# Performance work log

Hardware: AMD Instinct MI355X
Metric: run time of the kernel (lower is better)

Reference implementation:

```python
import jax, jax.numpy as jnp
import numpy as np

N_NODES = 100000
N_EDGES = 1600000
DROP_P = 0.5  # F.dropout default, training=True by default in the source
LRELU_SLOPE = 0.01
EPS = 1e-12


def setup_inputs() -> dict:
    key = jax.random.key(0)
    ks = jax.random.split(key, 8)
    x = jax.random.normal(ks[0], (N_NODES, 64), dtype=jnp.float32)
    edge_index = jax.random.randint(ks[1], (2, N_EDGES), 0, N_NODES, dtype=jnp.int64)
    s = 1.0 / np.sqrt(64)
    W1_l = jax.random.uniform(ks[2], (64, 32), jnp.float32, -s, s)
    W1_r = jax.random.uniform(ks[3], (64, 32), jnp.float32, -s, s)
    b1 = jnp.zeros((32,), jnp.float32)
    s2 = 1.0 / np.sqrt(32)
    W2_l = jax.random.uniform(ks[4], (32, 64), jnp.float32, -s2, s2)
    W2_r = jax.random.uniform(ks[5], (32, 64), jnp.float32, -s2, s2)
    b2 = jnp.zeros((64,), jnp.float32)
    return {"x": x, "edge_index": edge_index, "W1_l": W1_l, "b1": b1,
            "W1_r": W1_r, "W2_l": W2_l, "b2": b2, "W2_r": W2_r}


def _sage_conv(x, src, dst, W_l, b, W_r, n):
    # mean aggregation of source features onto destinations (PyG SAGEConv)
    msg = x[src]                                                 # [E, d]
    agg = jax.ops.segment_sum(msg, dst, num_segments=n)          # [N, d]
    cnt = jax.ops.segment_sum(jnp.ones((src.shape[0],), x.dtype), dst, num_segments=n)
    mean = agg / jnp.maximum(cnt, 1.0)[:, None]
    return mean @ W_l + b + x @ W_r


def _dropout(x, key):
    keep = jax.random.bernoulli(key, 1.0 - DROP_P, x.shape)
    return jnp.where(keep, x / (1.0 - DROP_P), 0.0).astype(x.dtype)


def reference(x, edge_index, W1_l, b1, W1_r, W2_l, b2, W2_r):
    n = x.shape[0]
    src, dst = edge_index[0], edge_index[1]
    dk = jax.random.split(jax.random.key(42), 2)
    h = _sage_conv(x, src, dst, W1_l, b1, W1_r, n)
    h = jax.nn.leaky_relu(h, LRELU_SLOPE)
    h = _dropout(h, dk[0])
    h = _sage_conv(h, src, dst, W2_l, b2, W2_r, n)
    h = _dropout(h, dk[1])
    norm = jnp.sqrt(jnp.sum(h * h, axis=1, keepdims=True))
    return h / jnp.maximum(norm, EPS)
```

## Files before the change

### kernel.cpp

```cpp
#include <hip/hip_runtime.h>

#define N_NODES 100000
#define N_EDGES 1600000
#define NPB 32
#define NB (N_NODES / NPB)
#define CAP 704
#define NCC 49
#define CAPA 34816
#define NFB 64
#define BPC 16
#define N16 (N_NODES * 16)
#define GHB 6250
#define M1W 50000
#define M2W 100000

typedef float v2f __attribute__((ext_vector_type(2)));

#define PIN4(v) asm volatile("" : "+v"(v.x), "+v"(v.y), "+v"(v.z), "+v"(v.w))

struct U2 { unsigned a, b; };

__host__ __device__ constexpr U2 tf2x32(unsigned k0, unsigned k1, unsigned c0, unsigned c1) {
  unsigned ks2 = k0 ^ k1 ^ 0x1BD11BDAu;
  unsigned x0 = c0 + k0, x1 = c1 + k1;
#define TFR(r) { x0 += x1; x1 = (x1 << (r)) | (x1 >> (32 - (r))); x1 ^= x0; }
  TFR(13) TFR(15) TFR(26) TFR(6)
  x0 += k1;  x1 += ks2 + 1u;
  TFR(17) TFR(29) TFR(16) TFR(24)
  x0 += ks2; x1 += k0 + 2u;
  TFR(13) TFR(15) TFR(26) TFR(6)
  x0 += k0;  x1 += k1 + 3u;
  TFR(17) TFR(29) TFR(16) TFR(24)
  x0 += k1;  x1 += ks2 + 4u;
  TFR(13) TFR(15) TFR(26) TFR(6)
  x0 += ks2; x1 += k0 + 5u;
#undef TFR
  return U2{x0, x1};
}

constexpr U2 DK0 = tf2x32(0u, 42u, 0u, 0u);
constexpr U2 DK1 = tf2x32(0u, 42u, 0u, 1u);

__device__ __forceinline__ bool keep_bit(unsigned k0, unsigned k1, unsigned j) {
  U2 w = tf2x32(k0, k1, 0u, j);
  return ((w.a ^ w.b) >> 31) == 0u;
}

__device__ __forceinline__ unsigned short f2bf(float f) {
  unsigned u = __float_as_uint(f);
  u += 0x7FFFu + ((u >> 16) & 1u);
  return (unsigned short)(u >> 16);
}
__device__ __forceinline__ v2f up2(unsigned r) {
  v2f v;
  v.x = __uint_as_float(r << 16);
  v.y = __uint_as_float(r & 0xFFFF0000u);
  return v;
}

__device__ __forceinline__ float4 ldcol(const float* __restrict__ W, int i,
                                        int lane, int ld) {
  float4 v;
  v.x = W[(i * 4 + 0) * ld + lane];
  v.y = W[(i * 4 + 1) * ld + lane];
  v.z = W[(i * 4 + 2) * ld + lane];
  v.w = W[(i * 4 + 3) * ld + lane];
  return v;
}

__global__ __launch_bounds__(256) void k_mask(unsigned long long* __restrict__ msk) {
  int w = (int)((blockIdx.x * blockDim.x + threadIdx.x) >> 6);
  int lane = threadIdx.x & 63;
  int nw = (int)((gridDim.x * blockDim.x) >> 6);
  for (; w < M1W + M2W; w += nw) {
    unsigned k0, k1, j;
    if (w < M1W) { k0 = DK0.a; k1 = DK0.b; j = (unsigned)w * 64u + (unsigned)lane; }
    else { k0 = DK1.a; k1 = DK1.b; j = (unsigned)(w - M1W) * 64u + (unsigned)lane; }
    unsigned long long bits = __ballot(keep_bit(k0, k1, j));
    if (lane == 0) msk[w] = bits;
  }
}

__global__ __launch_bounds__(256, 4) void k_transform1(
    const float* __restrict__ x, const float* __restrict__ Wl,
    const float* __restrict__ Wr, unsigned short* __restrict__ xlbh,
    float* __restrict__ xr) {
  __shared__ __align__(16) float rv[2][4][64];
  int lane = threadIdx.x & 63;
  int wv = (threadIdx.x >> 6) & 3;
  const float* W = (lane < 32) ? Wl : Wr;
  int c = lane & 31;
  float4 V0 = ldcol(W, 0, c, 32);   PIN4(V0);
  float4 V1 = ldcol(W, 1, c, 32);   PIN4(V1);
  float4 V2 = ldcol(W, 2, c, 32);   PIN4(V2);
  float4 V3 = ldcol(W, 3, c, 32);   PIN4(V3);
  float4 V4 = ldcol(W, 4, c, 32);   PIN4(V4);
  float4 V5 = ldcol(W, 5, c, 32);   PIN4(V5);
  float4 V6 = ldcol(W, 6, c, 32);   PIN4(V6);
  float4 V7 = ldcol(W, 7, c, 32);   PIN4(V7);
  float4 V8 = ldcol(W, 8, c, 32);   PIN4(V8);
  float4 V9 = ldcol(W, 9, c, 32);   PIN4(V9);
  float4 V10 = ldcol(W, 10, c, 32); PIN4(V10);
  float4 V11 = ldcol(W, 11, c, 32); PIN4(V11);
  float4 V12 = ldcol(W, 12, c, 32); PIN4(V12);
  float4 V13 = ldcol(W, 13, c, 32); PIN4(V13);
  float4 V14 = ldcol(W, 14, c, 32); PIN4(V14);
  float4 V15 = ldcol(W, 15, c, 32); PIN4(V15);
  int wid0 = (int)((blockIdx.x * blockDim.x + threadIdx.x) >> 6);
  int wstride = (int)((gridDim.x * blockDim.x) >> 6);
  float xv = x[wid0 * 64 + lane];
  int b = 0;
  for (int wid = wid0; wid < N_NODES; wid += wstride) {
    rv[b][wv][lane] = xv;
    int nxt = wid + wstride;
    if (nxt < N_NODES) xv = x[nxt * 64 + lane];
    asm volatile("s_waitcnt lgkmcnt(0)" ::: "memory");
    const float* rb = &rv[b][wv][0];
    v2f s0 = {0.f, 0.f}, s1 = {0.f, 0.f};
#define TST(Vi, i) { \
    float4 r = *(const float4*)(rb + (i) * 4); \
    v2f w0; w0.x = Vi.x; w0.y = Vi.y; \
    v2f w1; w1.x = Vi.z; w1.y = Vi.w; \
    v2f p0; p0.x = r.x; p0.y = r.y; \
    v2f p1; p1.x = r.z; p1.y = r.w; \
    s0 += p0 * w0; s1 += p1 * w1; }
    TST(V0, 0)  TST(V1, 1)  TST(V2, 2)  TST(V3, 3)
    TST(V4, 4)  TST(V5, 5)  TST(V6, 6)  TST(V7, 7)
    TST(V8, 8)  TST(V9, 9)  TST(V10, 10) TST(V11, 11)
    TST(V12, 12) TST(V13, 13) TST(V14, 14) TST(V15, 15)
#undef TST
    float s = (s0.x + s0.y) + (s1.x + s1.y);
    if (lane < 32) xlbh[(size_t)(c >> 4) * N16 + wid * 16 + (c & 15)] = f2bf(s);
    else           xr[wid * 32 + c] = s;
    b ^= 1;
  }
}

__global__ __launch_bounds__(256) void k_binA(
    const int* __restrict__ src, const int* __restrict__ dst,
    int* __restrict__ curA, unsigned* __restrict__ bufA) {
  __shared__ int hist[NCC];
  __shared__ int offsL[NCC + 1];
  __shared__ int baseL[NCC];
  __shared__ int place[NCC];
  __shared__ unsigned stag[2048];
  __shared__ unsigned char cellb[2048];
  int t = threadIdx.x;
  for (long long start = (long long)blockIdx.x * 2048; start < N_EDGES;
       start += (long long)gridDim.x * 2048) {
    int n = (int)min((long long)2048, (long long)N_EDGES - start);
    for (int i = t; i < NCC; i += 256) hist[i] = 0;
    __syncthreads();
    unsigned pv[8]; int pc[8];
#pragma unroll
    for (int i = 0; i < 8; ++i) {
      int idx = t + i * 256;
      if (idx < n) {
        int d = dst[start + idx];
        int s = src[start + idx];
        int cc = d >> 11;
        pc[i] = cc;
        pv[i] = (unsigned)s | ((unsigned)(d & 2047) << 17);
        atomicAdd(&hist[cc], 1);
      } else pc[i] = -1;
    }
    __syncthreads();
    if (t < 64) {
      int lane = t;
      int v = (lane < NCC) ? hist[lane] : 0;
      int x = v;
#pragma unroll
      for (int o = 1; o < 64; o <<= 1) {
        int y = __shfl_up(x, o, 64);
        if (lane >= o) x += y;
      }
      if (lane < NCC) {
        offsL[lane] = x - v;
        place[lane] = 0;
        if (v > 0) baseL[lane] = atomicAdd(&curA[lane], v);
      }
      if (lane == NCC - 1) offsL[NCC] = x;
    }
    __syncthreads();
#pragma unroll
    for (int i = 0; i < 8; ++i) {
      if (pc[i] >= 0) {
        int p = atomicAdd(&place[pc[i]], 1);
        int sl = offsL[pc[i]] + p;
        stag[sl] = pv[i];
        cellb[sl] = (unsigned char)pc[i];
      }
    }
    __syncthreads();
    for (int s2 = t; s2 < n; s2 += 256) {
      int cell = cellb[s2];
      int pos = baseL[cell] + (s2 - offsL[cell]);
      if (pos < CAPA) bufA[(size_t)cell * CAPA + pos] = stag[s2];
    }
    __syncthreads();
  }
}

__global__ __launch_bounds__(256) void k_binB(
    const unsigned* __restrict__ bufA, const int* __restrict__ curA,
    int* __restrict__ cur, unsigned* __restrict__ buf) {
  __shared__ int hist[NFB];
  __shared__ int offsL[NFB + 1];
  __shared__ int baseL[NFB];
  __shared__ int place[NFB];
  __shared__ unsigned stag[2048];
  __shared__ unsigned char cellb[2048];
  int cellc = blockIdx.x / BPC;
  int slice = blockIdx.x % BPC;
  int t = threadIdx.x;
  int cnt = min(curA[cellc], CAPA);
  const unsigned* in = bufA + (size_t)cellc * CAPA;
  for (int start = slice * 2048; start < cnt; start += BPC * 2048) {
    int n = min(2048, cnt - start);
    for (int i = t; i < NFB; i += 256) hist[i] = 0;
    __syncthreads();
    unsigned pv[8]; int pb[8];
#pragma unroll
    for (int i = 0; i < 8; ++i) {
      int idx = t + i * 256;
      if (idx < n) {
        unsigned w = in[start + idx];
        int dlow = (int)(w >> 17);
        int fb = dlow >> 5;
        pb[i] = fb;
        pv[i] = (w & 0x1FFFFu) | ((unsigned)(dlow & 31) << 17);
        atomicAdd(&hist[fb], 1);
      } else pb[i] = -1;
    }
    __syncthreads();
    if (t < 64) {
      int lane = t;
      int v = hist[lane];
      int x = v;
#pragma unroll
      for (int o = 1; o < 64; o <<= 1) {
        int y = __shfl_up(x, o, 64);
        if (lane >= o) x += y;
      }
      offsL[lane] = x - v;
      place[lane] = 0;
      if (v > 0) baseL[lane] = atomicAdd(&cur[cellc * NFB + lane], v);
      if (lane == 63) offsL[NFB] = x;
    }
    __syncthreads();
#pragma unroll
    for (int i = 0; i < 8; ++i) {
      if (pb[i] >= 0) {
        int p = atomicAdd(&place[pb[i]], 1);
        int sl = offsL[pb[i]] + p;
        stag[sl] = pv[i];
        cellb[sl] = (unsigned char)pb[i];
      }
    }
    __syncthreads();
    for (int s2 = t; s2 < n; s2 += 256) {
      int fb = cellb[s2];
      int pos = baseL[fb] + (s2 - offsL[fb]);
      if (pos < CAP) buf[(size_t)(cellc * NFB + fb) * CAP + pos] = stag[s2];
    }
    __syncthreads();
  }
}

__global__ __launch_bounds__(1024) void k_bscan(
    const int* __restrict__ cur, int* __restrict__ bbase) {
  __shared__ int warp_sums[16];
  __shared__ int s_running;
  int t = threadIdx.x;
  int lane = t & 63, w = t >> 6;
  if (t == 0) s_running = 0;
  __syncthreads();
  for (int base = 0; base < NB; base += 1024) {
    int i = base + t;
    int v = (i < NB) ? min(cur[i], CAP) : 0;
    int x = v;
#pragma unroll
    for (int o = 1; o < 64; o <<= 1) {
      int y = __shfl_up(x, o, 64);
      if (lane >= o) x += y;
    }
    if (lane == 63) warp_sums[w] = x;
    __syncthreads();
    if (w == 0) {
      int ws = (lane < 16) ? warp_sums[lane] : 0;
#pragma unroll
      for (int o = 1; o < 16; o <<= 1) {
        int y = __shfl_up(ws, o, 64);
        if (lane >= o) ws += y;
      }
      if (lane < 16) warp_sums[lane] = ws;
    }
    __syncthreads();
    int incl = x + (w > 0 ? warp_sums[w - 1] : 0);
    int excl = s_running + incl - v;
    if (i < NB) bbase[i] = excl;
    __syncthreads();
    if (t == 1023) s_running += incl;
    __syncthreads();
  }
}

__global__ __launch_bounds__(256) void k_bfill(
    const unsigned* __restrict__ buf, const int* __restrict__ cur,
    const int* __restrict__ bbase, int* __restrict__ deg,
    int* __restrict__ offs, int* __restrict__ eidx) {
  __shared__ int ncnt[NPB];
  __shared__ int ncur[NPB];
  __shared__ unsigned sbuf[CAP];
  int b = blockIdx.x, t = threadIdx.x;
  if (t < NPB) ncnt[t] = 0;
  __syncthreads();
  int nb = min(cur[b], CAP);
  const unsigned* bb = buf + (size_t)b * CAP;
  for (int slot = t; slot < nb; slot += 256) {
    unsigned w = bb[slot];
    sbuf[slot] = w;
    atomicAdd(&ncnt[w >> 17], 1);
  }
  __syncthreads();
  if (t < 64) {
    int lane = t;
    int c = (lane < NPB) ? ncnt[lane] : 0;
    int x = c;
#pragma unroll
    for (int o = 1; o < 32; o <<= 1) {
      int y = __shfl_up(x, o, 64);
      if (lane >= o) x += y;
    }
    if (lane < NPB) {
      int excl = x - c;
      ncur[lane] = excl;
      int gn = b * NPB + lane;
      deg[gn] = c;
      offs[gn] = bbase[b] + excl;
    }
  }
  __syncthreads();
  int base = bbase[b];
  for (int slot = t; slot < nb; slot += 256) {
    unsigned w = sbuf[slot];
    int p = atomicAdd(&ncur[w >> 17], 1);
    eidx[base + p] = (int)(w & 0x1FFFF);
  }
}

__global__ __launch_bounds__(256) void k_gather1(
    const unsigned short* __restrict__ xlbh, const float* __restrict__ xr,
    const int* __restrict__ offs, const int* __restrict__ deg,
    const int* __restrict__ eidx, const float* __restrict__ b1,
    const unsigned long long* __restrict__ msk1,
    unsigned short* __restrict__ hpbh) {
  int bb = blockIdx.x;
  int G = 0, nb = bb;
  if (nb >= GHB) { G = 1; nb -= GHB; }
  int tid = threadIdx.x;
  int lane = tid & 63;
  int node = nb * 16 + (tid >> 4);
  int g = (tid >> 2) & 3;
  int ch = tid & 3;
  int c = tid & 15;
  int col = G * 16 + c;
  int off = offs[node];
  int dg = deg[node];
  float xr_v = xr[node * 32 + col];
  float b1_v = b1[col];
  unsigned jj = (unsigned)(node * 32 + col);
  unsigned long long mw = msk1[jj >> 6];
  const uint2* H = (const uint2*)(xlbh + (size_t)G * N16);
  v2f acc01 = {0.f, 0.f}, acc23 = {0.f, 0.f};
  int k = 0;
  for (; k + 8 <= dg; k += 8) {
    int s0 = eidx[off + k + g];
    int s1 = eidx[off + k + 4 + g];
    uint2 r0 = H[s0 * 4 + ch];
    uint2 r1 = H[s1 * 4 + ch];
    acc01 += up2(r0.x); acc23 += up2(r0.y);
    acc01 += up2(r1.x); acc23 += up2(r1.y);
  }
  for (; k < dg; k += 4) {
    if (k + g < dg) {
      int s = eidx[off + k + g];
      uint2 r = H[s * 4 + ch];
      acc01 += up2(r.x); acc23 += up2(r.y);
    }
  }
  float a0 = acc01.x, a1 = acc01.y, a2 = acc23.x, a3 = acc23.y;
  a0 += __shfl_xor(a0, 4, 64); a0 += __shfl_xor(a0, 8, 64);
  a1 += __shfl_xor(a1, 4, 64); a1 += __shfl_xor(a1, 8, 64);
  a2 += __shfl_xor(a2, 4, 64); a2 += __shfl_xor(a2, 8, 64);
  a3 += __shfl_xor(a3, 4, 64); a3 += __shfl_xor(a3, 8, 64);
  int srcl = (lane & 48) + (c >> 2);
  float t0 = __shfl(a0, srcl, 64);
  float t1 = __shfl(a1, srcl, 64);
  float t2 = __shfl(a2, srcl, 64);
  float t3 = __shfl(a3, srcl, 64);
  int sub = lane & 3;
  float val = (sub == 0) ? t0 : (sub == 1) ? t1 : (sub == 2) ? t2 : t3;
  float inv = 1.0f / fmaxf((float)dg, 1.0f);
  float v = val * inv + b1_v + xr_v;
  v = (v > 0.f) ? v : 0.01f * v;
  float h = ((mw >> (jj & 63)) & 1ull) ? 2.0f * v : 0.0f;
  hpbh[(size_t)G * N16 + node * 16 + c] = f2bf(h);
}

__global__ __launch_bounds__(256) void k_gather2(
    const unsigned short* __restrict__ hpbh, const int* __restrict__ offs,
    const int* __restrict__ deg, const int* __restrict__ eidx,
    float* __restrict__ aggh) {
  int bb = blockIdx.x;
  int G = 0, nb = bb;
  if (nb >= GHB) { G = 1; nb -= GHB; }
  int tid = threadIdx.x;
  int lane = tid & 63;
  int node = nb * 16 + (tid >> 4);
  int g = (tid >> 2) & 3;
  int ch = tid & 3;
  int c = tid & 15;
  int off = offs[node];
  int dg = deg[node];
  const uint2* H = (const uint2*)(hpbh + (size_t)G * N16);
  v2f acc01 = {0.f, 0.f}, acc23 = {0.f, 0.f};
  int k = 0;
  for (; k + 8 <= dg; k += 8) {
    int s0 = eidx[off + k + g];
    int s1 = eidx[off + k + 4 + g];
    uint2 r0 = H[s0 * 4 + ch];
    uint2 r1 = H[s1 * 4 + ch];
    acc01 += up2(r0.x); acc23 += up2(r0.y);
    acc01 += up2(r1.x); acc23 += up2(r1.y);
  }
  for (; k < dg; k += 4) {
    if (k + g < dg) {
      int s = eidx[off + k + g];
      uint2 r = H[s * 4 + ch];
      acc01 += up2(r.x); acc23 += up2(r.y);
    }
  }
  float a0 = acc01.x, a1 = acc01.y, a2 = acc23.x, a3 = acc23.y;
  a0 += __shfl_xor(a0, 4, 64); a0 += __shfl_xor(a0, 8, 64);
  a1 += __shfl_xor(a1, 4, 64); a1 += __shfl_xor(a1, 8, 64);
  a2 += __shfl_xor(a2, 4, 64); a2 += __shfl_xor(a2, 8, 64);
  a3 += __shfl_xor(a3, 4, 64); a3 += __shfl_xor(a3, 8, 64);
  int srcl = (lane & 48) + (c >> 2);
  float t0 = __shfl(a0, srcl, 64);
  float t1 = __shfl(a1, srcl, 64);
  float t2 = __shfl(a2, srcl, 64);
  float t3 = __shfl(a3, srcl, 64);
  int sub = lane & 3;
  float val = (sub == 0) ? t0 : (sub == 1) ? t1 : (sub == 2) ? t2 : t3;
  float inv = 1.0f / fmaxf((float)dg, 1.0f);
  aggh[(size_t)G * N16 + node * 16 + c] = val * inv;
}

__global__ __launch_bounds__(256, 4) void k_out2(
    const unsigned short* __restrict__ hpbh, const float* __restrict__ aggh,
    const float* __restrict__ W2l, const float* __restrict__ b2,
    const float* __restrict__ W2r, const unsigned long long* __restrict__ msk2,
    float* __restrict__ out) {
  __shared__ __align__(16) float rv[2][4][64];
  int lane = threadIdx.x & 63;
  int wv = (threadIdx.x >> 6) & 3;
  float4 L0 = ldcol(W2l, 0, lane, 64); PIN4(L0);
  float4 L1 = ldcol(W2l, 1, lane, 64); PIN4(L1);
  float4 L2 = ldcol(W2l, 2, lane, 64); PIN4(L2);
  float4 L3 = ldcol(W2l, 3, lane, 64); PIN4(L3);
  float4 L4 = ldcol(W2l, 4, lane, 64); PIN4(L4);
  float4 L5 = ldcol(W2l, 5, lane, 64); PIN4(L5);
  float4 L6 = ldcol(W2l, 6, lane, 64); PIN4(L6);
  float4 L7 = ldcol(W2l, 7, lane, 64); PIN4(L7);
  float4 R0 = ldcol(W2r, 0, lane, 64); PIN4(R0);
  float4 R1 = ldcol(W2r, 1, lane, 64); PIN4(R1);
  float4 R2 = ldcol(W2r, 2, lane, 64); PIN4(R2);
  float4 R3 = ldcol(W2r, 3, lane, 64); PIN4(R3);
  float4 R4 = ldcol(W2r, 4, lane, 64); PIN4(R4);
  float4 R5 = ldcol(W2r, 5, lane, 64); PIN4(R5);
  float4 R6 = ldcol(W2r, 6, lane, 64); PIN4(R6);
  float4 R7 = ldcol(W2r, 7, lane, 64); PIN4(R7);
  float bias = b2[lane];
  int wid0 = (int)((blockIdx.x * blockDim.x + threadIdx.x) >> 6);
  int wstride = (int)((gridDim.x * blockDim.x) >> 6);
  float4 pa; uint2 ph;
#define PRELOAD(widx) { \
  if (lane < 8) { \
    const float* ap = aggh + ((lane < 4) ? 0 : (size_t)N16) + (size_t)(widx) * 16 + (lane & 3) * 4; \
    pa = *(const float4*)ap; \
  } else if (lane < 16) { \
    const uint2* Hp = (const uint2*)(hpbh + ((lane < 12) ? 0 : (size_t)N16)); \
    ph = Hp[(size_t)(widx) * 4 + (lane & 3)]; \
  } }
  PRELOAD(wid0);
  int b = 0;
  for (int wid = wid0; wid < N_NODES; wid += wstride) {
    if (lane < 8) {
      *(float4*)&rv[b][wv][lane * 4] = pa;
    } else if (lane < 16) {
      v2f lo = up2(ph.x), hi = up2(ph.y);
      float4 v; v.x = lo.x; v.y = lo.y; v.z = hi.x; v.w = hi.y;
      *(float4*)&rv[b][wv][32 + (lane - 8) * 4] = v;
    }
    int nxt = wid + wstride;
    if (nxt < N_NODES) PRELOAD(nxt);
    unsigned long long mw = msk2[wid];
    asm volatile("s_waitcnt lgkmcnt(0)" ::: "memory");
    const float* rb = &rv[b][wv][0];
    v2f sa = {0.f, 0.f}, sb = {0.f, 0.f};
#define GST(Li, Ri, i) { \
    float4 r1 = *(const float4*)(rb + (i) * 4); \
    float4 r2 = *(const float4*)(rb + 32 + (i) * 4); \
    v2f w0; w0.x = Li.x; w0.y = Li.y; \
    v2f w1; w1.x = Li.z; w1.y = Li.w; \
    v2f u0; u0.x = Ri.x; u0.y = Ri.y; \
    v2f u1; u1.x = Ri.z; u1.y = Ri.w; \
    v2f p0; p0.x = r1.x; p0.y = r1.y; \
    v2f p1; p1.x = r1.z; p1.y = r1.w; \
    v2f q0; q0.x = r2.x; q0.y = r2.y; \
    v2f q1; q1.x = r2.z; q1.y = r2.w; \
    sa += p0 * w0; sa += p1 * w1; \
    sb += q0 * u0; sb += q1 * u1; }
    GST(L0, R0, 0) GST(L1, R1, 1) GST(L2, R2, 2) GST(L3, R3, 3)
    GST(L4, R4, 4) GST(L5, R5, 5) GST(L6, R6, 6) GST(L7, R7, 7)
#undef GST
    float v = (sa.x + sa.y) + (sb.x + sb.y) + bias;
    float d = ((mw >> lane) & 1ull) ? 2.0f * v : 0.0f;
    float ss = d * d;
#pragma unroll
    for (int o = 32; o > 0; o >>= 1) ss += __shfl_xor(ss, o, 64);
    float scale = 1.0f / fmaxf(sqrtf(ss), 1e-12f);
    out[(size_t)wid * 64 + lane] = d * scale;
    b ^= 1;
  }
#undef PRELOAD
}

extern "C" void kernel_launch(void* const* d_in, const int* in_sizes, int n_in,
                              void* d_out, int out_size, void* d_ws, size_t ws_size,
                              hipStream_t stream) {
  const float* x   = (const float*)d_in[0];
  const int*   ei  = (const int*)d_in[1];
  const float* W1l = (const float*)d_in[2];
  const float* b1  = (const float*)d_in[3];
  const float* W1r = (const float*)d_in[4];
  const float* W2l = (const float*)d_in[5];
  const float* b2  = (const float*)d_in[6];
  const float* W2r = (const float*)d_in[7];
  float* out = (float*)d_out;

  const int* src = ei;
  const int* dst = ei + N_EDGES;

  const size_t F32 = (size_t)N_NODES * 32;
  char* w = (char*)d_ws;
  unsigned* bufA = (unsigned*)w;
  float* xr      = (float*)w;
  float* aggh    = (float*)w;
  w += F32 * sizeof(float);
  unsigned* buf  = (unsigned*)w;
  unsigned short* xlbh = (unsigned short*)w;
  unsigned short* hpbh = xlbh + 2 * (size_t)N16;
  w += F32 * 2 * sizeof(unsigned short);
  int* curA  = (int*)w; w += NCC * sizeof(int);
  int* cur   = (int*)w; w += NB * sizeof(int);
  int* bbase = (int*)w; w += NB * sizeof(int);
  int* deg   = (int*)w; w += N_NODES * sizeof(int);
  int* offs  = (int*)w; w += N_NODES * sizeof(int);
  int* eidx  = (int*)w; w += (size_t)N_EDGES * sizeof(int);
  unsigned long long* msk = (unsigned long long*)w;

  hipMemsetAsync(curA, 0, (size_t)(NCC + NB) * sizeof(int), stream);

  k_mask<<<2048, 256, 0, stream>>>(msk);
  k_binA<<<(N_EDGES + 2047) / 2048, 256, 0, stream>>>(src, dst, curA, bufA);
  k_binB<<<NCC * BPC, 256, 0, stream>>>(bufA, curA, cur, buf);
  k_bscan<<<1, 1024, 0, stream>>>(cur, bbase);
  k_bfill<<<NB, 256, 0, stream>>>(buf, cur, bbase, deg, offs, eidx);

  k_transform1<<<1024, 256, 0, stream>>>(x, W1l, W1r, xlbh, xr);
  k_gather1<<<2 * GHB, 256, 0, stream>>>(xlbh, xr, offs, deg, eidx, b1, msk, hpbh);
  k_gather2<<<2 * GHB, 256, 0, stream>>>(hpbh, offs, deg, eidx, aggh);
  k_out2<<<1024, 256, 0, stream>>>(hpbh, aggh, W2l, b2, W2r, msk + M1W, out);
}
```

Before: 285.9 us.

## Map one thread per node in output kernel with transposed weights

Rewrites the final layer kernel so each thread handles a whole node, holding its 64 input features in registers and computing each output column from a pre-transposed weight copy (built inside the mask kernel). The goal is to remove LDS staging, barriers/waitcnts and cross-lane reductions. In exchange, it recomputes all dot products twice (once for the norm, once for output), has strided per-thread memory access, and raises register pressure.

```diff
diff --git a/kernel.cpp b/kernel.cpp
--- a/kernel.cpp
+++ b/kernel.cpp
@@ -68,7 +68,16 @@
   return v;
 }
 
-__global__ __launch_bounds__(256) void k_mask(unsigned long long* __restrict__ msk) {
+__global__ __launch_bounds__(256) void k_mask(
+    unsigned long long* __restrict__ msk,
+    const float* __restrict__ W2l, const float* __restrict__ W2r,
+    float* __restrict__ wt) {
+  int bid = blockIdx.x, tid = threadIdx.x;
+  if (bid == 2) {
+    for (int i = tid; i < 2048; i += 256) { int c = i >> 5, k = i & 31; wt[i] = W2l[k * 64 + c]; }
+  } else if (bid == 3) {
+    for (int i = tid; i < 2048; i += 256) { int c = i >> 5, k = i & 31; wt[2048 + i] = W2r[k * 64 + c]; }
+  }
   int w = (int)((blockIdx.x * blockDim.x + threadIdx.x) >> 6);
   int lane = threadIdx.x & 63;
   int nw = (int)((gridDim.x * blockDim.x) >> 6);
@@ -459,82 +468,73 @@
 
 __global__ __launch_bounds__(256, 4) void k_out2(
     const unsigned short* __restrict__ hpbh, const float* __restrict__ aggh,
-    const float* __restrict__ W2l, const float* __restrict__ b2,
-    const float* __restrict__ W2r, const unsigned long long* __restrict__ msk2,
+    const float* __restrict__ W2lT, const float* __restrict__ b2,
+    const float* __restrict__ W2rT, const unsigned long long* __restrict__ msk2,
     float* __restrict__ out) {
-  __shared__ __align__(16) float rv[2][4][64];
-  int lane = threadIdx.x & 63;
-  int wv = (threadIdx.x >> 6) & 3;
-  float4 L0 = ldcol(W2l, 0, lane, 64); PIN4(L0);
-  float4 L1 = ldcol(W2l, 1, lane, 64); PIN4(L1);
-  float4 L2 = ldcol(W2l, 2, lane, 64); PIN4(L2);
-  float4 L3 = ldcol(W2l, 3, lane, 64); PIN4(L3);
-  float4 L4 = ldcol(W2l, 4, lane, 64); PIN4(L4);
-  float4 L5 = ldcol(W2l, 5, lane, 64); PIN4(L5);
-  float4 L6 = ldcol(W2l, 6, lane, 64); PIN4(L6);
-  float4 L7 = ldcol(W2l, 7, lane, 64); PIN4(L7);
-  float4 R0 = ldcol(W2r, 0, lane, 64); PIN4(R0);
-  float4 R1 = ldcol(W2r, 1, lane, 64); PIN4(R1);
-  float4 R2 = ldcol(W2r, 2, lane, 64); PIN4(R2);
-  float4 R3 = ldcol(W2r, 3, lane, 64); PIN4(R3);
-  float4 R4 = ldcol(W2r, 4, lane, 64); PIN4(R4);
-  float4 R5 = ldcol(W2r, 5, lane, 64); PIN4(R5);
-  float4 R6 = ldcol(W2r, 6, lane, 64); PIN4(R6);
-  float4 R7 = ldcol(W2r, 7, lane, 64); PIN4(R7);
-  float bias = b2[lane];
-  int wid0 = (int)((blockIdx.x * blockDim.x + threadIdx.x) >> 6);
-  int wstride = (int)((gridDim.x * blockDim.x) >> 6);
-  float4 pa; uint2 ph;
-#define PRELOAD(widx) { \
-  if (lane < 8) { \
-    const float* ap = aggh + ((lane < 4) ? 0 : (size_t)N16) + (size_t)(widx) * 16 + (lane & 3) * 4; \
-    pa = *(const float4*)ap; \
-  } else if (lane < 16) { \
-    const uint2* Hp = (const uint2*)(hpbh + ((lane < 12) ? 0 : (size_t)N16)); \
-    ph = Hp[(size_t)(widx) * 4 + (lane & 3)]; \
-  } }
-  PRELOAD(wid0);
-  int b = 0;
-  for (int wid = wid0; wid < N_NODES; wid += wstride) {
-    if (lane < 8) {
-      *(float4*)&rv[b][wv][lane * 4] = pa;
-    } else if (lane < 16) {
-      v2f lo = up2(ph.x), hi = up2(ph.y);
-      float4 v; v.x = lo.x; v.y = lo.y; v.z = hi.x; v.w = hi.y;
-      *(float4*)&rv[b][wv][32 + (lane - 8) * 4] = v;
-    }
-    int nxt = wid + wstride;
-    if (nxt < N_NODES) PRELOAD(nxt);
-    unsigned long long mw = msk2[wid];
-    asm volatile("s_waitcnt lgkmcnt(0)" ::: "memory");
-    const float* rb = &rv[b][wv][0];
-    v2f sa = {0.f, 0.f}, sb = {0.f, 0.f};
-#define GST(Li, Ri, i) { \
-    float4 r1 = *(const float4*)(rb + (i) * 4); \
-    float4 r2 = *(const float4*)(rb + 32 + (i) * 4); \
-    v2f w0; w0.x = Li.x; w0.y = Li.y; \
-    v2f w1; w1.x = Li.z; w1.y = Li.w; \
-    v2f u0; u0.x = Ri.x; u0.y = Ri.y; \
-    v2f u1; u1.x = Ri.z; u1.y = Ri.w; \
-    v2f p0; p0.x = r1.x; p0.y = r1.y; \
-    v2f p1; p1.x = r1.z; p1.y = r1.w; \
-    v2f q0; q0.x = r2.x; q0.y = r2.y; \
-    v2f q1; q1.x = r2.z; q1.y = r2.w; \
-    sa += p0 * w0; sa += p1 * w1; \
-    sb += q0 * u0; sb += q1 * u1; }
-    GST(L0, R0, 0) GST(L1, R1, 1) GST(L2, R2, 2) GST(L3, R3, 3)
-    GST(L4, R4, 4) GST(L5, R5, 5) GST(L6, R6, 6) GST(L7, R7, 7)
-#undef GST
-    float v = (sa.x + sa.y) + (sb.x + sb.y) + bias;
-    float d = ((mw >> lane) & 1ull) ? 2.0f * v : 0.0f;
-    float ss = d * d;
-#pragma unroll
-    for (int o = 32; o > 0; o >>= 1) ss += __shfl_xor(ss, o, 64);
-    float scale = 1.0f / fmaxf(sqrtf(ss), 1e-12f);
-    out[(size_t)wid * 64 + lane] = d * scale;
-    b ^= 1;
-  }
-#undef PRELOAD
+  int node = blockIdx.x * 256 + threadIdx.x;
+  if (node >= N_NODES) return;
+  const float4* a0p = (const float4*)(aggh + (size_t)node * 16);
+  const float4* a1p = (const float4*)(aggh + (size_t)N16 + (size_t)node * 16);
+  float4 A0 = a0p[0], A1 = a0p[1], A2 = a0p[2], A3 = a0p[3];
+  float4 A4 = a1p[0], A5 = a1p[1], A6 = a1p[2], A7 = a1p[3];
+  const uint4* h0p = (const uint4*)(hpbh + (size_t)node * 16);
+  const uint4* h1p = (const uint4*)(hpbh + (size_t)N16 + (size_t)node * 16);
+  uint4 ua = h0p[0], ub = h0p[1], uc = h1p[0], ud = h1p[1];
+  float4 H0, H1, H2, H3, H4, H5, H6, H7;
+  { v2f t0 = up2(ua.x), t1 = up2(ua.y); H0 = make_float4(t0.x, t0.y, t1.x, t1.y); }
+  { v2f t0 = up2(ua.z), t1 = up2(ua.w); H1 = make_float4(t0.x, t0.y, t1.x, t1.y); }
+  { v2f t0 = up2(ub.x), t1 = up2(ub.y); H2 = make_float4(t0.x, t0.y, t1.x, t1.y); }
+  { v2f t0 = up2(ub.z), t1 = up2(ub.w); H3 = make_float4(t0.x, t0.y, t1.x, t1.y); }
+  { v2f t0 = up2(uc.x), t1 = up2(uc.y); H4 = make_float4(t0.x, t0.y, t1.x, t1.y); }
+  { v2f t0 = up2(uc.z), t1 = up2(uc.w); H5 = make_float4(t0.x, t0.y, t1.x, t1.y); }
+  { v2f t0 = up2(ud.x), t1 = up2(ud.y); H6 = make_float4(t0.x, t0.y, t1.x, t1.y); }
+  { v2f t0 = up2(ud.z), t1 = up2(ud.w); H7 = make_float4(t0.x, t0.y, t1.x, t1.y); }
+  unsigned long long mw = msk2[node];
+
+#define COL(J, DD) \
+  float DD; { \
+    const float4* wlp = (const float4*)(W2lT + (size_t)(J) * 32); \
+    const float4* wrp = (const float4*)(W2rT + (size_t)(J) * 32); \
+    float4 w0 = wlp[0], w1 = wlp[1], w2 = wlp[2], w3 = wlp[3]; \
+    float4 w4 = wlp[4], w5 = wlp[5], w6 = wlp[6], w7 = wlp[7]; \
+    float4 u0 = wrp[0], u1 = wrp[1], u2 = wrp[2], u3 = wrp[3]; \
+    float4 u4 = wrp[4], u5 = wrp[5], u6 = wrp[6], u7 = wrp[7]; \
+    float s = b2[J]; \
+    s += A0.x * w0.x + A0.y * w0.y + A0.z * w0.z + A0.w * w0.w; \
+    s += A1.x * w1.x + A1.y * w1.y + A1.z * w1.z + A1.w * w1.w; \
+    s += A2.x * w2.x + A2.y * w2.y + A2.z * w2.z + A2.w * w2.w; \
+    s += A3.x * w3.x + A3.y * w3.y + A3.z * w3.z + A3.w * w3.w; \
+    s += A4.x * w4.x + A4.y * w4.y + A4.z * w4.z + A4.w * w4.w; \
+    s += A5.x * w5.x + A5.y * w5.y + A5.z * w5.z + A5.w * w5.w; \
+    s += A6.x * w6.x + A6.y * w6.y + A6.z * w6.z + A6.w * w6.w; \
+    s += A7.x * w7.x + A7.y * w7.y + A7.z * w7.z + A7.w * w7.w; \
+    s += H0.x * u0.x + H0.y * u0.y + H0.z * u0.z + H0.w * u0.w; \
+    s += H1.x * u1.x + H1.y * u1.y + H1.z * u1.z + H1.w * u1.w; \
+    s += H2.x * u2.x + H2.y * u2.y + H2.z * u2.z + H2.w * u2.w; \
+    s += H3.x * u3.x + H3.y * u3.y + H3.z * u3.z + H3.w * u3.w; \
+    s += H4.x * u4.x + H4.y * u4.y + H4.z * u4.z + H4.w * u4.w; \
+    s += H5.x * u5.x + H5.y * u5.y + H5.z * u5.z + H5.w * u5.w; \
+    s += H6.x * u6.x + H6.y * u6.y + H6.z * u6.z + H6.w * u6.w; \
+    s += H7.x * u7.x + H7.y * u7.y + H7.z * u7.z + H7.w * u7.w; \
+    DD = ((mw >> (J)) & 1ull) ? 2.0f * s : 0.0f; \
+  }
+
+  float ss = 0.f;
+  for (int j = 0; j < 64; ++j) {
+    COL(j, dd);
+    ss += dd * dd;
+  }
+  float scale = 1.0f / fmaxf(sqrtf(ss), 1e-12f);
+  float4* op = (float4*)(out + (size_t)node * 64);
+  for (int j4 = 0; j4 < 16; ++j4) {
+    int j = j4 * 4;
+    COL(j + 0, d0);
+    COL(j + 1, d1);
+    COL(j + 2, d2);
+    COL(j + 3, d3);
+    op[j4] = make_float4(d0 * scale, d1 * scale, d2 * scale, d3 * scale);
+  }
+#undef COL
 }
 
 extern "C" void kernel_launch(void* const* d_in, const int* in_sizes, int n_in,
@@ -570,10 +570,14 @@
   int* offs  = (int*)w; w += N_NODES * sizeof(int);
   int* eidx  = (int*)w; w += (size_t)N_EDGES * sizeof(int);
   unsigned long long* msk = (unsigned long long*)w;
+  w += (size_t)(M1W + M2W) * sizeof(unsigned long long);
+  float* wt = (float*)w;
+  float* W2lT = wt;
+  float* W2rT = wt + 2048;
 
   hipMemsetAsync(curA, 0, (size_t)(NCC + NB) * sizeof(int), stream);
 
-  k_mask<<<2048, 256, 0, stream>>>(msk);
+  k_mask<<<2048, 256, 0, stream>>>(msk, W2l, W2r, wt);
   k_binA<<<(N_EDGES + 2047) / 2048, 256, 0, stream>>>(src, dst, curA, bufA);
   k_binB<<<NCC * BPC, 256, 0, stream>>>(bufA, curA, cur, buf);
   k_bscan<<<1, 1024, 0, stream>>>(cur, bbase);
@@ -582,5 +586,5 @@
   k_transform1<<<1024, 256, 0, stream>>>(x, W1l, W1r, xlbh, xr);
   k_gather1<<<2 * GHB, 256, 0, stream>>>(xlbh, xr, offs, deg, eidx, b1, msk, hpbh);
   k_gather2<<<2 * GHB, 256, 0, stream>>>(hpbh, offs, deg, eidx, aggh);
-  k_out2<<<1024, 256, 0, stream>>>(hpbh, aggh, W2l, b2, W2r, msk + M1W, out);
-}
+  k_out2<<<(N_NODES + 255) / 256, 256, 0, stream>>>(hpbh, aggh, W2lT, b2, W2rT, msk + M1W, out);
+}
```

New measurement: 327.0 us. +14.4%, slower.
